# Optimization experiments

Measured on AMD Instinct MI355X. Metric: run time of the kernel, lower is better.

## Reference

```python
import jax, jax.numpy as jnp
import numpy as np

N = 50000      # nodes
E = 800000     # edges (before self loops)
F_IN = 50      # PPI num_features
H = 4          # heads
C = 64         # hidden per head
NC = 121       # PPI num_classes
NEG_SLOPE = 0.2


def setup_inputs() -> dict:
    key = jax.random.key(0)
    ks = jax.random.split(key, 20)
    p = lambda k, shape: (jax.random.normal(k, shape, jnp.float32) * 0.1)
    x0 = jax.random.normal(ks[0], (N, F_IN), jnp.float32)
    edge_index = jax.random.randint(ks[1], (2, E), 0, N, dtype=jnp.int64)
    return dict(
        x0=x0, edge_index=edge_index,
        W1=p(ks[2], (F_IN, H * C)), as1=p(ks[3], (H, C)), ad1=p(ks[4], (H, C)),
        res1=p(ks[5], (F_IN, H * C)), b1=jnp.zeros((H * C,), jnp.float32),
        W2=p(ks[6], (H * C, H * C)), as2=p(ks[7], (H, C)), ad2=p(ks[8], (H, C)),
        res2=p(ks[9], (H * C, H * C)), b2=jnp.zeros((H * C,), jnp.float32),
        W3=p(ks[10], (H * C, H * NC)), as3=p(ks[11], (H, NC)), ad3=p(ks[12], (H, NC)),
        res3=p(ks[13], (H * C, NC)), b3=jnp.zeros((NC,), jnp.float32),
    )


def _gat(x, src, dst, W, a_src, a_dst, resW, b, concat):
    """PyG-style GATConv with residual, self loops already in (src, dst)."""
    n = x.shape[0]
    heads, outc = a_src.shape
    h = (x @ W).reshape(n, heads, outc)                 # [N,H,C]
    al_s = (h * a_src).sum(-1)                          # [N,H]
    al_d = (h * a_dst).sum(-1)                          # [N,H]
    e = jax.nn.leaky_relu(al_s[src] + al_d[dst], NEG_SLOPE)  # [E,H]
    m = jax.ops.segment_max(e, dst, num_segments=n)     # stable softmax per dst
    ex = jnp.exp(e - m[dst])
    denom = jax.ops.segment_sum(ex, dst, num_segments=n)
    alpha = ex / denom[dst]                             # [E,H]
    out = jax.ops.segment_sum(h[src] * alpha[:, :, None], dst, num_segments=n)  # [N,H,C]
    out = out.reshape(n, heads * outc) if concat else out.mean(axis=1)
    return out + x @ resW + b


def reference(x0, edge_index,
              W1, as1, ad1, res1, b1,
              W2, as2, ad2, res2, b2,
              W3, as3, ad3, res3, b3):
    n = x0.shape[0]
    loop = jnp.arange(n, dtype=edge_index.dtype)        # add self loops (PyG default)
    src = jnp.concatenate([edge_index[0], loop])
    dst = jnp.concatenate([edge_index[1], loop])
    x1 = jax.nn.relu(_gat(x0, src, dst, W1, as1, ad1, res1, b1, True))
    x2 = jax.nn.relu(_gat(x1, src, dst, W2, as2, ad2, res2, b2, True))
    x3 = _gat(x2, src, dst, W3, as3, ad3, res3, b3, False)
    return x3
```

## Files before the change

kernel.cpp:

```cpp
#include <hip/hip_runtime.h>

#define NNODES 50000
#define NEDGES 800000
#define NTOT   (NEDGES + NNODES)
#define F_IN   50
#define KPAD1  64
#define HEADS  4
#define C1     64
#define HC1    256
#define NC     121
#define K1S    320
#define K3S    1280
#define N2S    512

typedef unsigned short ushort_t;
typedef __attribute__((ext_vector_type(4))) unsigned short ushort4_t;
typedef __attribute__((ext_vector_type(8))) unsigned short ushort8;
typedef __attribute__((ext_vector_type(8))) __bf16 bf16x8;
typedef __attribute__((ext_vector_type(4))) float f32x4;
typedef __attribute__((ext_vector_type(4))) int int4_t;

__device__ __forceinline__ ushort_t f2bf(float f) {
    union { float f; unsigned int u; } v; v.f = f;
    unsigned int u = v.u;
    return (ushort_t)((u + 0x7fffu + ((u >> 16) & 1u)) >> 16);
}
__device__ __forceinline__ float bf2f(ushort_t s) {
    union { unsigned int u; float f; } v; v.u = ((unsigned int)s) << 16;
    return v.f;
}
__device__ __forceinline__ float lrelu(float x) { return x > 0.f ? x : 0.2f * x; }
__device__ __forceinline__ f32x4 cvt4(ushort4_t v) {
    f32x4 r; r[0] = bf2f(v.x); r[1] = bf2f(v.y); r[2] = bf2f(v.z); r[3] = bf2f(v.w);
    return r;
}
__device__ __forceinline__ void wave_lds_sync() {
    asm volatile("s_waitcnt lgkmcnt(0)" ::: "memory");
}

__global__ void count_kernel(const int* __restrict__ ei, int* __restrict__ cnt) {
    int i = blockIdx.x * blockDim.x + threadIdx.x;
    if (i >= NTOT) return;
    int d = (i < NEDGES) ? ei[NEDGES + i] : (i - NEDGES);
    if ((unsigned)d >= NNODES) d = 0;
    atomicAdd(&cnt[d], 1);
}

#define SCB 256
__global__ __launch_bounds__(SCB)
void scan1_kernel(const int* __restrict__ cnt, int* __restrict__ incl,
                  int* __restrict__ bsums, int n) {
    __shared__ int buf[SCB];
    int b = blockIdx.x, tid = threadIdx.x;
    int i = b * SCB + tid;
    int v = (i < n) ? cnt[i] : 0;
    buf[tid] = v;
    __syncthreads();
    for (int off = 1; off < SCB; off <<= 1) {
        int t = (tid >= off) ? buf[tid - off] : 0;
        __syncthreads();
        buf[tid] += t;
        __syncthreads();
    }
    if (i < n) incl[i] = buf[tid];
    if (tid == SCB - 1) bsums[b] = buf[tid];
}

__global__ __launch_bounds__(SCB)
void scan2_kernel(int* __restrict__ bsums, int nb) {
    __shared__ int buf[SCB];
    int tid = threadIdx.x;
    int v = (tid < nb) ? bsums[tid] : 0;
    buf[tid] = v;
    __syncthreads();
    for (int off = 1; off < SCB; off <<= 1) {
        int t = (tid >= off) ? buf[tid - off] : 0;
        __syncthreads();
        buf[tid] += t;
        __syncthreads();
    }
    if (tid < nb) bsums[tid] = buf[tid] - v;
}

__global__ __launch_bounds__(SCB)
void scan3_kernel(const int* __restrict__ cnt, const int* __restrict__ incl,
                  const int* __restrict__ bsums, int* __restrict__ row_ptr,
                  int* __restrict__ cursor, int n) {
    int b = blockIdx.x, tid = threadIdx.x;
    int i = b * SCB + tid;
    if (i >= n) return;
    int e = bsums[b] + incl[i] - cnt[i];
    row_ptr[i] = e; cursor[i] = e;
    if (i == n - 1) row_ptr[n] = NTOT;
}

__global__ void scatter_kernel(const int* __restrict__ ei, int* __restrict__ cursor,
                               int* __restrict__ csr_src) {
    int i = blockIdx.x * blockDim.x + threadIdx.x;
    if (i >= NTOT) return;
    int s, d;
    if (i < NEDGES) { s = ei[i]; d = ei[NEDGES + i]; }
    else            { s = d = i - NEDGES; }
    if ((unsigned)d >= NNODES) d = 0;
    if ((unsigned)s >= NNODES) s = 0;
    int pos = atomicAdd(&cursor[d], 1);
    csr_src[pos] = s;
}

#define SZ_A (NNODES * KPAD1)
#define SZ_B (HC1 * K1S)
#define SZ_C (N2S * HC1)
#define SZ_D (N2S)
#define SZ_E (NC * K3S)
#define SZ_F (KPAD1 * 4)
#define SZ_G (HC1 * 4)
#define PREP_TOTAL (SZ_A + SZ_B + SZ_C + SZ_D + SZ_E + 2 * SZ_F + 4 * SZ_G)

__global__ __launch_bounds__(256)
void prep_kernel(const float* __restrict__ x0,
                 const float* __restrict__ W1, const float* __restrict__ res1,
                 const float* __restrict__ W2, const float* __restrict__ res2,
                 const float* __restrict__ W3, const float* __restrict__ res3,
                 const float* __restrict__ as1, const float* __restrict__ ad1,
                 const float* __restrict__ as2, const float* __restrict__ ad2,
                 const float* __restrict__ as3, const float* __restrict__ ad3,
                 const float* __restrict__ b2,
                 ushort_t* __restrict__ x0b, ushort_t* __restrict__ Bt1,
                 ushort_t* __restrict__ Bt2, ushort_t* __restrict__ Bt3,
                 float* __restrict__ bias512,
                 float* __restrict__ w_as1, float* __restrict__ w_ad1,
                 float* __restrict__ w_as2, float* __restrict__ w_ad2,
                 float* __restrict__ w_as3, float* __restrict__ w_ad3) {
    int i = blockIdx.x * 256 + threadIdx.x;
    if (i < SZ_A) {
        int m = i >> 6, k = i & 63;
        x0b[i] = (k < F_IN) ? f2bf(x0[(size_t)m * F_IN + k]) : (ushort_t)0;
        return;
    }
    i -= SZ_A;
    if (i < SZ_B) {
        int c = i / K1S, kk = i - c * K1S;
        float v = 0.f;
        if (kk < 256) {
            int h = kk >> 6, k = kk & 63;
            if (k < F_IN && (c >> 6) == h) v = W1[(size_t)k * HC1 + c];
        } else {
            int k = kk - 256;
            if (k < F_IN) v = res1[(size_t)k * HC1 + c];
        }
        Bt1[i] = f2bf(v);
        return;
    }
    i -= SZ_B;
    if (i < SZ_C) {
        int c = i / HC1, k = i - c * HC1;
        float v = (c < HC1) ? W2[(size_t)k * HC1 + c] : res2[(size_t)k * HC1 + (c - HC1)];
        Bt2[i] = f2bf(v);
        return;
    }
    i -= SZ_C;
    if (i < SZ_D) {
        bias512[i] = (i < HC1) ? 0.f : b2[i - HC1];
        return;
    }
    i -= SZ_D;
    if (i < SZ_E) {
        int c = i / K3S, kk = i - c * K3S;
        float v;
        if (kk < 1024) {
            int h = kk >> 8, k = kk & 255;
            v = 0.25f * W3[(size_t)k * (HEADS * NC) + h * NC + c];
        } else {
            int k = kk - 1024;
            v = res3[(size_t)k * NC + c];
        }
        Bt3[i] = f2bf(v);
        return;
    }
    i -= SZ_E;
    if (i < 2 * SZ_F) {
        const float* a = (i < SZ_F) ? as1 : ad1;
        float* w = (i < SZ_F) ? w_as1 : w_ad1;
        int ii = (i < SZ_F) ? i : i - SZ_F;
        int k = ii >> 2, h = ii & 3;
        float s = 0.f;
        if (k < F_IN)
            for (int c = 0; c < C1; ++c) s += W1[(size_t)k * HC1 + h * C1 + c] * a[h * C1 + c];
        w[ii] = s;
        return;
    }
    i -= 2 * SZ_F;
    {
        int grp = i / SZ_G, ii = i - grp * SZ_G;
        int k = ii >> 2, h = ii & 3;
        float s = 0.f;
        if (grp < 2) {
            const float* a = grp ? ad2 : as2;
            for (int c = 0; c < C1; ++c) s += W2[(size_t)k * HC1 + h * C1 + c] * a[h * C1 + c];
            (grp ? w_ad2 : w_as2)[ii] = s;
        } else {
            const float* a = (grp == 3) ? ad3 : as3;
            for (int c = 0; c < NC; ++c) s += W3[(size_t)k * (HEADS * NC) + h * NC + c] * a[h * NC + c];
            ((grp == 3) ? w_ad3 : w_as3)[ii] = s;
        }
    }
}

#define BM 128
#define BN 128
#define BK 64
#define LDP (BK + 8)

__global__ __launch_bounds__(256)
void gemm_mfma_kernel(const ushort_t* __restrict__ A1, int lda1,
                      const ushort_t* __restrict__ A2, int lda2, int Ksplit,
                      const ushort_t* __restrict__ Bt, const float* __restrict__ bias,
                      float* __restrict__ Cf, ushort_t* __restrict__ Cb,
                      int M, int N, int K, int relu) {
    __shared__ ushort_t As[BM * LDP];
    __shared__ ushort_t Bs[BN * LDP];
    int tid = threadIdx.x;
    int lane = tid & 63;
    int wid = tid >> 6;
    int wm = (wid & 1) * 64, wn = (wid >> 1) * 64;
    int l15 = lane & 15;
    int q8 = (lane >> 4) * 8;
    int m0 = blockIdx.y * BM, n0 = blockIdx.x * BN;

    f32x4 acc[4][4] = {};

    for (int k0 = 0; k0 < K; k0 += BK) {
        #pragma unroll
        for (int it = 0; it < 4; ++it) {
            int c = tid + it * 256;
            int row = c >> 3, c8 = c & 7;
            int k = k0 + c8 * 8;
            ushort8 va = (ushort8)0;
            int gm = m0 + row;
            if (gm < M) {
                if (k < Ksplit) va = *(const ushort8*)&A1[(size_t)gm * lda1 + k];
                else            va = *(const ushort8*)&A2[(size_t)gm * lda2 + (k - Ksplit)];
            }
            *(ushort8*)&As[row * LDP + c8 * 8] = va;
            ushort8 vb = (ushort8)0;
            int gn = n0 + row;
            if (gn < N) vb = *(const ushort8*)&Bt[(size_t)gn * K + k];
            *(ushort8*)&Bs[row * LDP + c8 * 8] = vb;
        }
        __syncthreads();
        #pragma unroll
        for (int kk = 0; kk < BK; kk += 32) {
            bf16x8 af[4], bfr[4];
            #pragma unroll
            for (int mi = 0; mi < 4; ++mi)
                af[mi] = *(const bf16x8*)&As[(wm + mi * 16 + l15) * LDP + kk + q8];
            #pragma unroll
            for (int ni = 0; ni < 4; ++ni)
                bfr[ni] = *(const bf16x8*)&Bs[(wn + ni * 16 + l15) * LDP + kk + q8];
            #pragma unroll
            for (int mi = 0; mi < 4; ++mi)
                #pragma unroll
                for (int ni = 0; ni < 4; ++ni)
                    acc[mi][ni] = __builtin_amdgcn_mfma_f32_16x16x32_bf16(
                        af[mi], bfr[ni], acc[mi][ni], 0, 0, 0);
        }
        __syncthreads();
    }

    #pragma unroll
    for (int mi = 0; mi < 4; ++mi) {
        int mbase = m0 + wm + mi * 16 + (lane >> 4) * 4;
        #pragma unroll
        for (int ni = 0; ni < 4; ++ni) {
            int ncol = n0 + wn + ni * 16 + l15;
            if (ncol >= N) continue;
            float bv = bias ? bias[ncol] : 0.f;
            #pragma unroll
            for (int r = 0; r < 4; ++r) {
                int m = mbase + r;
                if (m >= M) continue;
                float v = acc[mi][ni][r] + bv;
                if (relu) v = fmaxf(v, 0.f);
                if (Cf) Cf[(size_t)m * N + ncol] = v;
                else    Cb[(size_t)m * N + ncol] = f2bf(v);
            }
        }
    }
}

__global__ __launch_bounds__(256)
void logits_gemv_kernel(const ushort_t* __restrict__ X, int K,
                        const float* __restrict__ w_as, const float* __restrict__ w_ad,
                        float* __restrict__ als, float* __restrict__ ald) {
    int wid = threadIdx.x >> 6, lane = threadIdx.x & 63;
    int n = blockIdx.x * 4 + wid;
    float ps[HEADS] = {}, pd[HEADS] = {};
    for (int k0 = lane * 4; k0 < K; k0 += 256) {
        ushort4_t xv = *(const ushort4_t*)&X[(size_t)n * K + k0];
        float x[4] = {bf2f(xv.x), bf2f(xv.y), bf2f(xv.z), bf2f(xv.w)};
        #pragma unroll
        for (int j = 0; j < 4; ++j) {
            #pragma unroll
            for (int h = 0; h < HEADS; ++h) {
                ps[h] += x[j] * w_as[(k0 + j) * 4 + h];
                pd[h] += x[j] * w_ad[(k0 + j) * 4 + h];
            }
        }
    }
    #pragma unroll
    for (int off = 32; off; off >>= 1)
        #pragma unroll
        for (int h = 0; h < HEADS; ++h) {
            ps[h] += __shfl_xor(ps[h], off);
            pd[h] += __shfl_xor(pd[h], off);
        }
    if (lane == 0)
        #pragma unroll
        for (int h = 0; h < HEADS; ++h) {
            als[n * HEADS + h] = ps[h];
            ald[n * HEADS + h] = pd[h];
        }
}

#define E_CHUNK_NOMAX(ROWBYTES)                                               \
    int i = base + lane;                                                      \
    int nv = end - base; if (nv > 64) nv = 64;                                \
    if (i < end) {                                                            \
        int s = csr_src[i];                                                   \
        soffw[lane] = s * (ROWBYTES);                                         \
        f32x4 av = *(const f32x4*)&als[s * 4];                                \
        f32x4 e;                                                              \
        _Pragma("unroll")                                                     \
        for (int h = 0; h < HEADS; ++h) {                                     \
            e[h] = __expf(lrelu(av[h] + aldd[h]));                            \
            den4[h] += e[h];                                                  \
        }                                                                     \
        *(f32x4*)&sew[lane * 4] = e;                                          \
    }                                                                         \
    wave_lds_sync();

#define DEN_REDUCE                                                            \
    _Pragma("unroll")                                                         \
    for (int off = 32; off; off >>= 1)                                        \
        _Pragma("unroll")                                                     \
        for (int h = 0; h < HEADS; ++h)                                       \
            den4[h] += __shfl_xor(den4[h], off);

__global__ __launch_bounds__(256)
void agg1_kernel(const ushort_t* __restrict__ x0b,
                 const float* __restrict__ als, const float* __restrict__ ald,
                 const int* __restrict__ row_ptr, const int* __restrict__ csr_src,
                 ushort_t* __restrict__ aggx) {
    __shared__ int   soff[4][64];
    __shared__ float se[4][64 * 4];
    int wid = threadIdx.x >> 6, lane = threadIdx.x & 63;
    int d = blockIdx.x * 4 + wid;
    int* soffw = soff[wid];
    float* sew = se[wid];
    int beg = row_ptr[d], end = row_ptr[d + 1];
    f32x4 aldd = *(const f32x4*)&ald[d * 4];
    f32x4 den4 = (f32x4)0.f;
    f32x4 acc  = (f32x4)0.f;
    int lb = lane * 2;
    for (int base = beg; base < end; base += 64) {
        E_CHUNK_NOMAX(KPAD1 * 2)
        int j = 0;
        for (; j + 4 <= nv; j += 4) {
            int4_t o = *(const int4_t*)&soffw[j];
            f32x4 e0 = *(const f32x4*)&sew[j * 4];
            f32x4 e1 = *(const f32x4*)&sew[(j + 1) * 4];
            f32x4 e2 = *(const f32x4*)&sew[(j + 2) * 4];
            f32x4 e3 = *(const f32x4*)&sew[(j + 3) * 4];
            float x0v = bf2f(*(const ushort_t*)((const char*)x0b + o.x + lb));
            float x1v = bf2f(*(const ushort_t*)((const char*)x0b + o.y + lb));
            float x2v = bf2f(*(const ushort_t*)((const char*)x0b + o.z + lb));
            float x3v = bf2f(*(const ushort_t*)((const char*)x0b + o.w + lb));
            acc += e0 * x0v + e1 * x1v + e2 * x2v + e3 * x3v;
        }
        for (; j < nv; ++j) {
            int o = soffw[j];
            f32x4 e = *(const f32x4*)&sew[j * 4];
            float xv = bf2f(*(const ushort_t*)((const char*)x0b + o + lb));
            acc += e * xv;
        }
        wave_lds_sync();
    }
    DEN_REDUCE
    #pragma unroll
    for (int h = 0; h < HEADS; ++h)
        aggx[(size_t)d * HC1 + h * 64 + lane] = f2bf(acc[h] / den4[h]);
}

__global__ __launch_bounds__(256)
void agg2_kernel(const ushort_t* __restrict__ comb,
                 const float* __restrict__ als, const float* __restrict__ ald,
                 const int* __restrict__ row_ptr, const int* __restrict__ csr_src,
                 const float* __restrict__ w_as3, const float* __restrict__ w_ad3,
                 ushort_t* __restrict__ xnext,
                 float* __restrict__ als3, float* __restrict__ ald3) {
    __shared__ int   soff[4][64];
    __shared__ float se[4][64 * 4];
    int wid = threadIdx.x >> 6, lane = threadIdx.x & 63;
    int d = blockIdx.x * 4 + wid;
    int* soffw = soff[wid];
    float* sew = se[wid];
    int hh = lane >> 4;
    int beg = row_ptr[d], end = row_ptr[d + 1];
    f32x4 aldd = *(const f32x4*)&ald[d * 4];
    f32x4 den4 = (f32x4)0.f;
    f32x4 acc  = (f32x4)0.f;
    int lb = lane * 8;
    for (int base = beg; base < end; base += 64) {
        E_CHUNK_NOMAX(N2S * 2)
        int j = 0;
        for (; j + 4 <= nv; j += 4) {
            int4_t o = *(const int4_t*)&soffw[j];
            float e0 = sew[j * 4 + hh], e1 = sew[(j + 1) * 4 + hh];
            float e2 = sew[(j + 2) * 4 + hh], e3 = sew[(j + 3) * 4 + hh];
            f32x4 x0v = cvt4(*(const ushort4_t*)((const char*)comb + o.x + lb));
            f32x4 x1v = cvt4(*(const ushort4_t*)((const char*)comb + o.y + lb));
            f32x4 x2v = cvt4(*(const ushort4_t*)((const char*)comb + o.z + lb));
            f32x4 x3v = cvt4(*(const ushort4_t*)((const char*)comb + o.w + lb));
            acc += e0 * x0v + e1 * x1v + e2 * x2v + e3 * x3v;
        }
        for (; j < nv; ++j) {
            int o = soffw[j];
            float e = sew[j * 4 + hh];
            acc += e * cvt4(*(const ushort4_t*)((const char*)comb + o + lb));
        }
        wave_lds_sync();
    }
    DEN_REDUCE
    float r = 1.f / den4[hh];
    ushort4_t rv = *(const ushort4_t*)&comb[(size_t)d * N2S + 256 + lane * 4];
    f32x4 resv = cvt4(rv);
    f32x4 vout;
    #pragma unroll
    for (int c = 0; c < 4; ++c) vout[c] = fmaxf(acc[c] * r + resv[c], 0.f);
    ushort4_t o4;
    o4.x = f2bf(vout[0]); o4.y = f2bf(vout[1]); o4.z = f2bf(vout[2]); o4.w = f2bf(vout[3]);
    *(ushort4_t*)&xnext[(size_t)d * HC1 + lane * 4] = o4;
    f32x4 ps = (f32x4)0.f, pd = (f32x4)0.f;
    #pragma unroll
    for (int j = 0; j < 4; ++j) {
        f32x4 wsj = *(const f32x4*)&w_as3[(lane * 4 + j) * 4];
        f32x4 wdj = *(const f32x4*)&w_ad3[(lane * 4 + j) * 4];
        ps += vout[j] * wsj;
        pd += vout[j] * wdj;
    }
    #pragma unroll
    for (int off = 32; off; off >>= 1) {
        #pragma unroll
        for (int h = 0; h < HEADS; ++h) {
            ps[h] += __shfl_xor(ps[h], off);
            pd[h] += __shfl_xor(pd[h], off);
        }
    }
    if (lane == 0) {
        *(f32x4*)&als3[d * 4] = ps;
        *(f32x4*)&ald3[d * 4] = pd;
    }
}

__global__ __launch_bounds__(256)
void agg3_kernel(const ushort_t* __restrict__ x2b,
                 const float* __restrict__ als, const float* __restrict__ ald,
                 const int* __restrict__ row_ptr, const int* __restrict__ csr_src,
                 ushort_t* __restrict__ aggx) {
    __shared__ int   soff[4][64];
    __shared__ float se[4][64 * 4];
    int wid = threadIdx.x >> 6, lane = threadIdx.x & 63;
    int d = blockIdx.x * 4 + wid;
    int* soffw = soff[wid];
    float* sew = se[wid];
    int beg = row_ptr[d], end = row_ptr[d + 1];
    f32x4 aldd = *(const f32x4*)&ald[d * 4];
    f32x4 den4 = (f32x4)0.f;
    f32x4 acc[HEADS] = {};
    int lb = lane * 8;
    for (int base = beg; base < end; base += 64) {
        E_CHUNK_NOMAX(HC1 * 2)
        int j = 0;
        for (; j + 4 <= nv; j += 4) {
            int4_t o = *(const int4_t*)&soffw[j];
            f32x4 e0 = *(const f32x4*)&sew[j * 4];
            f32x4 e1 = *(const f32x4*)&sew[(j + 1) * 4];
            f32x4 e2 = *(const f32x4*)&sew[(j + 2) * 4];
            f32x4 e3 = *(const f32x4*)&sew[(j + 3) * 4];
            f32x4 x0v = cvt4(*(const ushort4_t*)((const char*)x2b + o.x + lb));
            f32x4 x1v = cvt4(*(const ushort4_t*)((const char*)x2b + o.y + lb));
            f32x4 x2v = cvt4(*(const ushort4_t*)((const char*)x2b + o.z + lb));
            f32x4 x3v = cvt4(*(const ushort4_t*)((const char*)x2b + o.w + lb));
            #pragma unroll
            for (int h = 0; h < HEADS; ++h)
                acc[h] += e0[h] * x0v + e1[h] * x1v + e2[h] * x2v + e3[h] * x3v;
        }
        for (; j < nv; ++j) {
            int o = soffw[j];
            f32x4 e = *(const f32x4*)&sew[j * 4];
            f32x4 xv = cvt4(*(const ushort4_t*)((const char*)x2b + o + lb));
            #pragma unroll
            for (int h = 0; h < HEADS; ++h) acc[h] += e[h] * xv;
        }
        wave_lds_sync();
    }
    DEN_REDUCE
    #pragma unroll
    for (int h = 0; h < HEADS; ++h) {
        float rd = 1.f / den4[h];
        ushort4_t o4;
        o4.x = f2bf(acc[h][0] * rd); o4.y = f2bf(acc[h][1] * rd);
        o4.z = f2bf(acc[h][2] * rd); o4.w = f2bf(acc[h][3] * rd);
        *(ushort4_t*)&aggx[(size_t)d * 1024 + h * HC1 + lane * 4] = o4;
    }
}

extern "C" void kernel_launch(void* const* d_in, const int* in_sizes, int n_in,
                              void* d_out, int out_size, void* d_ws, size_t ws_size,
                              hipStream_t stream) {
    const float* x0   = (const float*)d_in[0];
    const int*   ei   = (const int*)d_in[1];
    const float* W1   = (const float*)d_in[2];
    const float* as1  = (const float*)d_in[3];
    const float* ad1  = (const float*)d_in[4];
    const float* res1 = (const float*)d_in[5];
    const float* b1   = (const float*)d_in[6];
    const float* W2   = (const float*)d_in[7];
    const float* as2  = (const float*)d_in[8];
    const float* ad2  = (const float*)d_in[9];
    const float* res2 = (const float*)d_in[10];
    const float* b2   = (const float*)d_in[11];
    const float* W3   = (const float*)d_in[12];
    const float* as3  = (const float*)d_in[13];
    const float* ad3  = (const float*)d_in[14];
    const float* res3 = (const float*)d_in[15];
    const float* b3   = (const float*)d_in[16];

    char* p = (char*)d_ws;
    auto alloc = [&](size_t bytes) -> void* {
        void* r = (void*)p;
        p += (bytes + 255) & ~(size_t)255;
        return r;
    };
    int*      cnt     = (int*)alloc((size_t)NNODES * 4);
    int*      incl    = (int*)alloc((size_t)NNODES * 4);
    int*      bsums   = (int*)alloc((size_t)SCB * 4);
    int*      row_ptr = (int*)alloc((size_t)(NNODES + 1) * 4);
    int*      cursor  = (int*)alloc((size_t)NNODES * 4);
    int*      csr_src = (int*)alloc((size_t)NTOT * 4);
    float*    als     = (float*)alloc((size_t)NNODES * HEADS * 4);
    float*    ald     = (float*)alloc((size_t)NNODES * HEADS * 4);
    float*    als3    = (float*)alloc((size_t)NNODES * HEADS * 4);
    float*    ald3    = (float*)alloc((size_t)NNODES * HEADS * 4);
    ushort_t* x0b     = (ushort_t*)alloc((size_t)NNODES * KPAD1 * 2);
    ushort_t* x2      = (ushort_t*)alloc((size_t)NNODES * HC1 * 2);
    ushort_t* Bt1     = (ushort_t*)alloc((size_t)HC1 * K1S * 2);
    ushort_t* Bt2     = (ushort_t*)alloc((size_t)N2S * HC1 * 2);
    float*    bias512 = (float*)alloc((size_t)N2S * 4);
    ushort_t* Bt3     = (ushort_t*)alloc((size_t)NC * K3S * 2);
    float*    w_as1   = (float*)alloc((size_t)KPAD1 * 4 * 4);
    float*    w_ad1   = (float*)alloc((size_t)KPAD1 * 4 * 4);
    float*    w_as2   = (float*)alloc((size_t)HC1 * 4 * 4);
    float*    w_ad2   = (float*)alloc((size_t)HC1 * 4 * 4);
    float*    w_as3   = (float*)alloc((size_t)HC1 * 4 * 4);
    float*    w_ad3   = (float*)alloc((size_t)HC1 * 4 * 4);
    char*     big     = (char*)alloc((size_t)NNODES * 1024 * 2);
    ushort_t* aggx1   = (ushort_t*)big;
    ushort_t* x1      = (ushort_t*)(big + (size_t)NNODES * HC1 * 2);
    ushort_t* comb    = (ushort_t*)(big + (size_t)NNODES * HC1 * 4);
    ushort_t* aggx3   = (ushort_t*)big;

    hipMemsetAsync(cnt, 0, (size_t)NNODES * 4, stream);

    int tb = 256;
    int nscan = (NNODES + SCB - 1) / SCB;
    count_kernel<<<(NTOT + tb - 1) / tb, tb, 0, stream>>>(ei, cnt);
    scan1_kernel<<<nscan, SCB, 0, stream>>>(cnt, incl, bsums, NNODES);
    scan2_kernel<<<1, SCB, 0, stream>>>(bsums, nscan);
    scan3_kernel<<<nscan, SCB, 0, stream>>>(cnt, incl, bsums, row_ptr, cursor, NNODES);
    scatter_kernel<<<(NTOT + tb - 1) / tb, tb, 0, stream>>>(ei, cursor, csr_src);

    prep_kernel<<<(PREP_TOTAL + 255) / 256, 256, 0, stream>>>(
        x0, W1, res1, W2, res2, W3, res3, as1, ad1, as2, ad2, as3, ad3, b2,
        x0b, Bt1, Bt2, Bt3, bias512, w_as1, w_ad1, w_as2, w_ad2, w_as3, w_ad3);

    auto gemm = [&](const ushort_t* A1, int lda1, const ushort_t* A2, int lda2, int Ksplit,
                    const ushort_t* Bt, const float* bias,
                    float* Cf, ushort_t* Cb, int M, int Nn, int K, int relu) {
        dim3 g((Nn + BN - 1) / BN, (M + BM - 1) / BM);
        gemm_mfma_kernel<<<g, 256, 0, stream>>>(A1, lda1, A2, lda2, Ksplit, Bt, bias,
                                                Cf, Cb, M, Nn, K, relu);
    };

    int nagg = NNODES / 4;

    logits_gemv_kernel<<<nagg, 256, 0, stream>>>(x0b, KPAD1, w_as1, w_ad1, als, ald);
    agg1_kernel<<<nagg, 256, 0, stream>>>(x0b, als, ald, row_ptr, csr_src, aggx1);
    gemm(aggx1, HC1, x0b, KPAD1, HC1, Bt1, b1, nullptr, x1, NNODES, HC1, K1S, 1);

    gemm(x1, HC1, x1, HC1, HC1, Bt2, bias512, nullptr, comb, NNODES, N2S, HC1, 0);
    logits_gemv_kernel<<<nagg, 256, 0, stream>>>(x1, HC1, w_as2, w_ad2, als, ald);
    agg2_kernel<<<nagg, 256, 0, stream>>>(comb, als, ald, row_ptr, csr_src,
                                          w_as3, w_ad3, x2, als3, ald3);

    agg3_kernel<<<nagg, 256, 0, stream>>>(x2, als3, ald3, row_ptr, csr_src, aggx3);
    gemm(aggx3, 1024, x2, HC1, 1024, Bt3, b3, (float*)d_out, nullptr, NNODES, NC, K3S, 0);
}
```

Baseline: 640.7 us.

## Fuse independent setup kernels and make aggregation kernels grid-stride persistent

New measurement: 659.9 us. 1.03x slower.

```diff
diff --git a/kernel.cpp b/kernel.cpp
--- a/kernel.cpp
+++ b/kernel.cpp
@@ -38,8 +38,8 @@
     asm volatile("s_waitcnt lgkmcnt(0)" ::: "memory");
 }
 
-__global__ void count_kernel(const int* __restrict__ ei, int* __restrict__ cnt) {
-    int i = blockIdx.x * blockDim.x + threadIdx.x;
+__device__ __forceinline__ void count_body(int i, const int* __restrict__ ei,
+                                           int* __restrict__ cnt) {
     if (i >= NTOT) return;
     int d = (i < NEDGES) ? ei[NEDGES + i] : (i - NEDGES);
     if ((unsigned)d >= NNODES) d = 0;
@@ -94,9 +94,9 @@
     if (i == n - 1) row_ptr[n] = NTOT;
 }
 
-__global__ void scatter_kernel(const int* __restrict__ ei, int* __restrict__ cursor,
-                               int* __restrict__ csr_src) {
-    int i = blockIdx.x * blockDim.x + threadIdx.x;
+__device__ __forceinline__ void scatter_body(int i, const int* __restrict__ ei,
+                                             int* __restrict__ cursor,
+                                             int* __restrict__ csr_src) {
     if (i >= NTOT) return;
     int s, d;
     if (i < NEDGES) { s = ei[i]; d = ei[NEDGES + i]; }
@@ -115,9 +115,11 @@
 #define SZ_F (KPAD1 * 4)
 #define SZ_G (HC1 * 4)
 #define PREP_TOTAL (SZ_A + SZ_B + SZ_C + SZ_D + SZ_E + 2 * SZ_F + 4 * SZ_G)
-
-__global__ __launch_bounds__(256)
-void prep_kernel(const float* __restrict__ x0,
+#define PREP_BLK ((PREP_TOTAL + 255) / 256)
+#define CNT_BLK  ((NTOT + 255) / 256)
+
+__device__ void prep_body(int i,
+                 const float* __restrict__ x0,
                  const float* __restrict__ W1, const float* __restrict__ res1,
                  const float* __restrict__ W2, const float* __restrict__ res2,
                  const float* __restrict__ W3, const float* __restrict__ res3,
@@ -131,7 +133,6 @@
                  float* __restrict__ w_as1, float* __restrict__ w_ad1,
                  float* __restrict__ w_as2, float* __restrict__ w_ad2,
                  float* __restrict__ w_as3, float* __restrict__ w_ad3) {
-    int i = blockIdx.x * 256 + threadIdx.x;
     if (i < SZ_A) {
         int m = i >> 6, k = i & 63;
         x0b[i] = (k < F_IN) ? f2bf(x0[(size_t)m * F_IN + k]) : (ushort_t)0;
@@ -203,6 +204,32 @@
             for (int c = 0; c < NC; ++c) s += W3[(size_t)k * (HEADS * NC) + h * NC + c] * a[h * NC + c];
             ((grp == 3) ? w_ad3 : w_as3)[ii] = s;
         }
+    }
+}
+
+__global__ __launch_bounds__(256)
+void prep_count_kernel(const float* __restrict__ x0,
+                 const float* __restrict__ W1, const float* __restrict__ res1,
+                 const float* __restrict__ W2, const float* __restrict__ res2,
+                 const float* __restrict__ W3, const float* __restrict__ res3,
+                 const float* __restrict__ as1, const float* __restrict__ ad1,
+                 const float* __restrict__ as2, const float* __restrict__ ad2,
+                 const float* __restrict__ as3, const float* __restrict__ ad3,
+                 const float* __restrict__ b2,
+                 ushort_t* __restrict__ x0b, ushort_t* __restrict__ Bt1,
+                 ushort_t* __restrict__ Bt2, ushort_t* __restrict__ Bt3,
+                 float* __restrict__ bias512,
+                 float* __restrict__ w_as1, float* __restrict__ w_ad1,
+                 float* __restrict__ w_as2, float* __restrict__ w_ad2,
+                 float* __restrict__ w_as3, float* __restrict__ w_ad3,
+                 const int* __restrict__ ei, int* __restrict__ cnt) {
+    int b = blockIdx.x;
+    if (b < PREP_BLK) {
+        prep_body(b * 256 + threadIdx.x, x0, W1, res1, W2, res2, W3, res3,
+                  as1, ad1, as2, ad2, as3, ad3, b2, x0b, Bt1, Bt2, Bt3,
+                  bias512, w_as1, w_ad1, w_as2, w_ad2, w_as3, w_ad3);
+    } else {
+        count_body((b - PREP_BLK) * 256 + threadIdx.x, ei, cnt);
     }
 }
 
@@ -288,12 +315,10 @@
     }
 }
 
-__global__ __launch_bounds__(256)
-void logits_gemv_kernel(const ushort_t* __restrict__ X, int K,
+__device__ __forceinline__ void gemv_body(int n, int lane,
+                        const ushort_t* __restrict__ X, int K,
                         const float* __restrict__ w_as, const float* __restrict__ w_ad,
                         float* __restrict__ als, float* __restrict__ ald) {
-    int wid = threadIdx.x >> 6, lane = threadIdx.x & 63;
-    int n = blockIdx.x * 4 + wid;
     float ps[HEADS] = {}, pd[HEADS] = {};
     for (int k0 = lane * 4; k0 < K; k0 += 256) {
         ushort4_t xv = *(const ushort4_t*)&X[(size_t)n * K + k0];
@@ -320,6 +345,28 @@
             als[n * HEADS + h] = ps[h];
             ald[n * HEADS + h] = pd[h];
         }
+}
+
+__global__ __launch_bounds__(256)
+void logits_gemv_kernel(const ushort_t* __restrict__ X, int K,
+                        const float* __restrict__ w_as, const float* __restrict__ w_ad,
+                        float* __restrict__ als, float* __restrict__ ald) {
+    gemv_body(blockIdx.x * 4 + (threadIdx.x >> 6), threadIdx.x & 63, X, K, w_as, w_ad, als, ald);
+}
+
+#define GEMV_BLK (NNODES / 4)
+__global__ __launch_bounds__(256)
+void scatter_gemv1_kernel(const int* __restrict__ ei, int* __restrict__ cursor,
+                          int* __restrict__ csr_src,
+                          const ushort_t* __restrict__ X,
+                          const float* __restrict__ w_as, const float* __restrict__ w_ad,
+                          float* __restrict__ als, float* __restrict__ ald) {
+    int b = blockIdx.x;
+    if (b < GEMV_BLK) {
+        gemv_body(b * 4 + (threadIdx.x >> 6), threadIdx.x & 63, X, KPAD1, w_as, w_ad, als, ald);
+    } else {
+        scatter_body((b - GEMV_BLK) * 256 + threadIdx.x, ei, cursor, csr_src);
+    }
 }
 
 #define E_CHUNK_NOMAX(ROWBYTES)                                               \
@@ -346,6 +393,9 @@
         for (int h = 0; h < HEADS; ++h)                                       \
             den4[h] += __shfl_xor(den4[h], off);
 
+#define AGG_BLOCKS 2048
+#define AGG_WAVES  (AGG_BLOCKS * 4)
+
 __global__ __launch_bounds__(256)
 void agg1_kernel(const ushort_t* __restrict__ x0b,
                  const float* __restrict__ als, const float* __restrict__ ald,
@@ -354,41 +404,42 @@
     __shared__ int   soff[4][64];
     __shared__ float se[4][64 * 4];
     int wid = threadIdx.x >> 6, lane = threadIdx.x & 63;
-    int d = blockIdx.x * 4 + wid;
     int* soffw = soff[wid];
     float* sew = se[wid];
-    int beg = row_ptr[d], end = row_ptr[d + 1];
-    f32x4 aldd = *(const f32x4*)&ald[d * 4];
-    f32x4 den4 = (f32x4)0.f;
-    f32x4 acc  = (f32x4)0.f;
     int lb = lane * 2;
-    for (int base = beg; base < end; base += 64) {
-        E_CHUNK_NOMAX(KPAD1 * 2)
-        int j = 0;
-        for (; j + 4 <= nv; j += 4) {
-            int4_t o = *(const int4_t*)&soffw[j];
-            f32x4 e0 = *(const f32x4*)&sew[j * 4];
-            f32x4 e1 = *(const f32x4*)&sew[(j + 1) * 4];
-            f32x4 e2 = *(const f32x4*)&sew[(j + 2) * 4];
-            f32x4 e3 = *(const f32x4*)&sew[(j + 3) * 4];
-            float x0v = bf2f(*(const ushort_t*)((const char*)x0b + o.x + lb));
-            float x1v = bf2f(*(const ushort_t*)((const char*)x0b + o.y + lb));
-            float x2v = bf2f(*(const ushort_t*)((const char*)x0b + o.z + lb));
-            float x3v = bf2f(*(const ushort_t*)((const char*)x0b + o.w + lb));
-            acc += e0 * x0v + e1 * x1v + e2 * x2v + e3 * x3v;
-        }
-        for (; j < nv; ++j) {
-            int o = soffw[j];
-            f32x4 e = *(const f32x4*)&sew[j * 4];
-            float xv = bf2f(*(const ushort_t*)((const char*)x0b + o + lb));
-            acc += e * xv;
-        }
-        wave_lds_sync();
-    }
-    DEN_REDUCE
-    #pragma unroll
-    for (int h = 0; h < HEADS; ++h)
-        aggx[(size_t)d * HC1 + h * 64 + lane] = f2bf(acc[h] / den4[h]);
+    for (int d = blockIdx.x * 4 + wid; d < NNODES; d += AGG_WAVES) {
+        int beg = row_ptr[d], end = row_ptr[d + 1];
+        f32x4 aldd = *(const f32x4*)&ald[d * 4];
+        f32x4 den4 = (f32x4)0.f;
+        f32x4 acc  = (f32x4)0.f;
+        for (int base = beg; base < end; base += 64) {
+            E_CHUNK_NOMAX(KPAD1 * 2)
+            int j = 0;
+            for (; j + 4 <= nv; j += 4) {
+                int4_t o = *(const int4_t*)&soffw[j];
+                f32x4 e0 = *(const f32x4*)&sew[j * 4];
+                f32x4 e1 = *(const f32x4*)&sew[(j + 1) * 4];
+                f32x4 e2 = *(const f32x4*)&sew[(j + 2) * 4];
+                f32x4 e3 = *(const f32x4*)&sew[(j + 3) * 4];
+                float x0v = bf2f(*(const ushort_t*)((const char*)x0b + o.x + lb));
+                float x1v = bf2f(*(const ushort_t*)((const char*)x0b + o.y + lb));
+                float x2v = bf2f(*(const ushort_t*)((const char*)x0b + o.z + lb));
+                float x3v = bf2f(*(const ushort_t*)((const char*)x0b + o.w + lb));
+                acc += e0 * x0v + e1 * x1v + e2 * x2v + e3 * x3v;
+            }
+            for (; j < nv; ++j) {
+                int o = soffw[j];
+                f32x4 e = *(const f32x4*)&sew[j * 4];
+                float xv = bf2f(*(const ushort_t*)((const char*)x0b + o + lb));
+                acc += e * xv;
+            }
+            wave_lds_sync();
+        }
+        DEN_REDUCE
+        #pragma unroll
+        for (int h = 0; h < HEADS; ++h)
+            aggx[(size_t)d * HC1 + h * 64 + lane] = f2bf(acc[h] / den4[h]);
+    }
 }
 
 __global__ __launch_bounds__(256)
@@ -401,64 +452,66 @@
     __shared__ int   soff[4][64];
     __shared__ float se[4][64 * 4];
     int wid = threadIdx.x >> 6, lane = threadIdx.x & 63;
-    int d = blockIdx.x * 4 + wid;
     int* soffw = soff[wid];
     float* sew = se[wid];
     int hh = lane >> 4;
-    int beg = row_ptr[d], end = row_ptr[d + 1];
-    f32x4 aldd = *(const f32x4*)&ald[d * 4];
-    f32x4 den4 = (f32x4)0.f;
-    f32x4 acc  = (f32x4)0.f;
     int lb = lane * 8;
-    for (int base = beg; base < end; base += 64) {
-        E_CHUNK_NOMAX(N2S * 2)
-        int j = 0;
-        for (; j + 4 <= nv; j += 4) {
-            int4_t o = *(const int4_t*)&soffw[j];
-            float e0 = sew[j * 4 + hh], e1 = sew[(j + 1) * 4 + hh];
-            float e2 = sew[(j + 2) * 4 + hh], e3 = sew[(j + 3) * 4 + hh];
-            f32x4 x0v = cvt4(*(const ushort4_t*)((const char*)comb + o.x + lb));
-            f32x4 x1v = cvt4(*(const ushort4_t*)((const char*)comb + o.y + lb));
-            f32x4 x2v = cvt4(*(const ushort4_t*)((const char*)comb + o.z + lb));
-            f32x4 x3v = cvt4(*(const ushort4_t*)((const char*)comb + o.w + lb));
-            acc += e0 * x0v + e1 * x1v + e2 * x2v + e3 * x3v;
-        }
-        for (; j < nv; ++j) {
-            int o = soffw[j];
-            float e = sew[j * 4 + hh];
-            acc += e * cvt4(*(const ushort4_t*)((const char*)comb + o + lb));
-        }
-        wave_lds_sync();
-    }
-    DEN_REDUCE
-    float r = 1.f / den4[hh];
-    ushort4_t rv = *(const ushort4_t*)&comb[(size_t)d * N2S + 256 + lane * 4];
-    f32x4 resv = cvt4(rv);
-    f32x4 vout;
-    #pragma unroll
-    for (int c = 0; c < 4; ++c) vout[c] = fmaxf(acc[c] * r + resv[c], 0.f);
-    ushort4_t o4;
-    o4.x = f2bf(vout[0]); o4.y = f2bf(vout[1]); o4.z = f2bf(vout[2]); o4.w = f2bf(vout[3]);
-    *(ushort4_t*)&xnext[(size_t)d * HC1 + lane * 4] = o4;
-    f32x4 ps = (f32x4)0.f, pd = (f32x4)0.f;
-    #pragma unroll
-    for (int j = 0; j < 4; ++j) {
-        f32x4 wsj = *(const f32x4*)&w_as3[(lane * 4 + j) * 4];
-        f32x4 wdj = *(const f32x4*)&w_ad3[(lane * 4 + j) * 4];
-        ps += vout[j] * wsj;
-        pd += vout[j] * wdj;
-    }
-    #pragma unroll
-    for (int off = 32; off; off >>= 1) {
-        #pragma unroll
-        for (int h = 0; h < HEADS; ++h) {
-            ps[h] += __shfl_xor(ps[h], off);
-            pd[h] += __shfl_xor(pd[h], off);
-        }
-    }
-    if (lane == 0) {
-        *(f32x4*)&als3[d * 4] = ps;
-        *(f32x4*)&ald3[d * 4] = pd;
+    for (int d = blockIdx.x * 4 + wid; d < NNODES; d += AGG_WAVES) {
+        int beg = row_ptr[d], end = row_ptr[d + 1];
+        f32x4 aldd = *(const f32x4*)&ald[d * 4];
+        f32x4 den4 = (f32x4)0.f;
+        f32x4 acc  = (f32x4)0.f;
+        for (int base = beg; base < end; base += 64) {
+            E_CHUNK_NOMAX(N2S * 2)
+            int j = 0;
+            for (; j + 4 <= nv; j += 4) {
+                int4_t o = *(const int4_t*)&soffw[j];
+                float e0 = sew[j * 4 + hh], e1 = sew[(j + 1) * 4 + hh];
+                float e2 = sew[(j + 2) * 4 + hh], e3 = sew[(j + 3) * 4 + hh];
+                f32x4 x0v = cvt4(*(const ushort4_t*)((const char*)comb + o.x + lb));
+                f32x4 x1v = cvt4(*(const ushort4_t*)((const char*)comb + o.y + lb));
+                f32x4 x2v = cvt4(*(const ushort4_t*)((const char*)comb + o.z + lb));
+                f32x4 x3v = cvt4(*(const ushort4_t*)((const char*)comb + o.w + lb));
+                acc += e0 * x0v + e1 * x1v + e2 * x2v + e3 * x3v;
+            }
+            for (; j < nv; ++j) {
+                int o = soffw[j];
+                float e = sew[j * 4 + hh];
+                acc += e * cvt4(*(const ushort4_t*)((const char*)comb + o + lb));
+            }
+            wave_lds_sync();
+        }
+        DEN_REDUCE
+        float r = 1.f / den4[hh];
+        ushort4_t rv = *(const ushort4_t*)&comb[(size_t)d * N2S + 256 + lane * 4];
+        f32x4 resv = cvt4(rv);
+        f32x4 vout;
+        #pragma unroll
+        for (int c = 0; c < 4; ++c) vout[c] = fmaxf(acc[c] * r + resv[c], 0.f);
+        ushort4_t o4;
+        o4.x = f2bf(vout[0]); o4.y = f2bf(vout[1]);
+        o4.z = f2bf(vout[2]); o4.w = f2bf(vout[3]);
+        *(ushort4_t*)&xnext[(size_t)d * HC1 + lane * 4] = o4;
+        f32x4 ps = (f32x4)0.f, pd = (f32x4)0.f;
+        #pragma unroll
+        for (int j = 0; j < 4; ++j) {
+            f32x4 wsj = *(const f32x4*)&w_as3[(lane * 4 + j) * 4];
+            f32x4 wdj = *(const f32x4*)&w_ad3[(lane * 4 + j) * 4];
+            ps += vout[j] * wsj;
+            pd += vout[j] * wdj;
+        }
+        #pragma unroll
+        for (int off = 32; off; off >>= 1) {
+            #pragma unroll
+            for (int h = 0; h < HEADS; ++h) {
+                ps[h] += __shfl_xor(ps[h], off);
+                pd[h] += __shfl_xor(pd[h], off);
+            }
+        }
+        if (lane == 0) {
+            *(f32x4*)&als3[d * 4] = ps;
+            *(f32x4*)&ald3[d * 4] = pd;
+        }
     }
 }
 
@@ -470,48 +523,49 @@
     __shared__ int   soff[4][64];
     __shared__ float se[4][64 * 4];
     int wid = threadIdx.x >> 6, lane = threadIdx.x & 63;
-    int d = blockIdx.x * 4 + wid;
     int* soffw = soff[wid];
     float* sew = se[wid];
-    int beg = row_ptr[d], end = row_ptr[d + 1];
-    f32x4 aldd = *(const f32x4*)&ald[d * 4];
-    f32x4 den4 = (f32x4)0.f;
-    f32x4 acc[HEADS] = {};
     int lb = lane * 8;
-    for (int base = beg; base < end; base += 64) {
-        E_CHUNK_NOMAX(HC1 * 2)
-        int j = 0;
-        for (; j + 4 <= nv; j += 4) {
-            int4_t o = *(const int4_t*)&soffw[j];
-            f32x4 e0 = *(const f32x4*)&sew[j * 4];
-            f32x4 e1 = *(const f32x4*)&sew[(j + 1) * 4];
-            f32x4 e2 = *(const f32x4*)&sew[(j + 2) * 4];
-            f32x4 e3 = *(const f32x4*)&sew[(j + 3) * 4];
-            f32x4 x0v = cvt4(*(const ushort4_t*)((const char*)x2b + o.x + lb));
-            f32x4 x1v = cvt4(*(const ushort4_t*)((const char*)x2b + o.y + lb));
-            f32x4 x2v = cvt4(*(const ushort4_t*)((const char*)x2b + o.z + lb));
-            f32x4 x3v = cvt4(*(const ushort4_t*)((const char*)x2b + o.w + lb));
-            #pragma unroll
-            for (int h = 0; h < HEADS; ++h)
-                acc[h] += e0[h] * x0v + e1[h] * x1v + e2[h] * x2v + e3[h] * x3v;
-        }
-        for (; j < nv; ++j) {
-            int o = soffw[j];
-            f32x4 e = *(const f32x4*)&sew[j * 4];
-            f32x4 xv = cvt4(*(const ushort4_t*)((const char*)x2b + o + lb));
-            #pragma unroll
-            for (int h = 0; h < HEADS; ++h) acc[h] += e[h] * xv;
-        }
-        wave_lds_sync();
-    }
-    DEN_REDUCE
-    #pragma unroll
-    for (int h = 0; h < HEADS; ++h) {
-        float rd = 1.f / den4[h];
-        ushort4_t o4;
-        o4.x = f2bf(acc[h][0] * rd); o4.y = f2bf(acc[h][1] * rd);
-        o4.z = f2bf(acc[h][2] * rd); o4.w = f2bf(acc[h][3] * rd);
-        *(ushort4_t*)&aggx[(size_t)d * 1024 + h * HC1 + lane * 4] = o4;
+    for (int d = blockIdx.x * 4 + wid; d < NNODES; d += AGG_WAVES) {
+        int beg = row_ptr[d], end = row_ptr[d + 1];
+        f32x4 aldd = *(const f32x4*)&ald[d * 4];
+        f32x4 den4 = (f32x4)0.f;
+        f32x4 acc[HEADS] = {};
+        for (int base = beg; base < end; base += 64) {
+            E_CHUNK_NOMAX(HC1 * 2)
+            int j = 0;
+            for (; j + 4 <= nv; j += 4) {
+                int4_t o = *(const int4_t*)&soffw[j];
+                f32x4 e0 = *(const f32x4*)&sew[j * 4];
+                f32x4 e1 = *(const f32x4*)&sew[(j + 1) * 4];
+                f32x4 e2 = *(const f32x4*)&sew[(j + 2) * 4];
+                f32x4 e3 = *(const f32x4*)&sew[(j + 3) * 4];
+                f32x4 x0v = cvt4(*(const ushort4_t*)((const char*)x2b + o.x + lb));
+                f32x4 x1v = cvt4(*(const ushort4_t*)((const char*)x2b + o.y + lb));
+                f32x4 x2v = cvt4(*(const ushort4_t*)((const char*)x2b + o.z + lb));
+                f32x4 x3v = cvt4(*(const ushort4_t*)((const char*)x2b + o.w + lb));
+                #pragma unroll
+                for (int h = 0; h < HEADS; ++h)
+                    acc[h] += e0[h] * x0v + e1[h] * x1v + e2[h] * x2v + e3[h] * x3v;
+            }
+            for (; j < nv; ++j) {
+                int o = soffw[j];
+                f32x4 e = *(const f32x4*)&sew[j * 4];
+                f32x4 xv = cvt4(*(const ushort4_t*)((const char*)x2b + o + lb));
+                #pragma unroll
+                for (int h = 0; h < HEADS; ++h) acc[h] += e[h] * xv;
+            }
+            wave_lds_sync();
+        }
+        DEN_REDUCE
+        #pragma unroll
+        for (int h = 0; h < HEADS; ++h) {
+            float rdv = 1.f / den4[h];
+            ushort4_t o4;
+            o4.x = f2bf(acc[h][0] * rdv); o4.y = f2bf(acc[h][1] * rdv);
+            o4.z = f2bf(acc[h][2] * rdv); o4.w = f2bf(acc[h][3] * rdv);
+            *(ushort4_t*)&aggx[(size_t)d * 1024 + h * HC1 + lane * 4] = o4;
+        }
     }
 }
 
@@ -572,17 +626,17 @@
 
     hipMemsetAsync(cnt, 0, (size_t)NNODES * 4, stream);
 
-    int tb = 256;
     int nscan = (NNODES + SCB - 1) / SCB;
-    count_kernel<<<(NTOT + tb - 1) / tb, tb, 0, stream>>>(ei, cnt);
+
+    prep_count_kernel<<<PREP_BLK + CNT_BLK, 256, 0, stream>>>(
+        x0, W1, res1, W2, res2, W3, res3, as1, ad1, as2, ad2, as3, ad3, b2,
+        x0b, Bt1, Bt2, Bt3, bias512, w_as1, w_ad1, w_as2, w_ad2, w_as3, w_ad3,
+        ei, cnt);
     scan1_kernel<<<nscan, SCB, 0, stream>>>(cnt, incl, bsums, NNODES);
     scan2_kernel<<<1, SCB, 0, stream>>>(bsums, nscan);
     scan3_kernel<<<nscan, SCB, 0, stream>>>(cnt, incl, bsums, row_ptr, cursor, NNODES);
-    scatter_kernel<<<(NTOT + tb - 1) / tb, tb, 0, stream>>>(ei, cursor, csr_src);
-
-    prep_kernel<<<(PREP_TOTAL + 255) / 256, 256, 0, stream>>>(
-        x0, W1, res1, W2, res2, W3, res3, as1, ad1, as2, ad2, as3, ad3, b2,
-        x0b, Bt1, Bt2, Bt3, bias512, w_as1, w_ad1, w_as2, w_ad2, w_as3, w_ad3);
+    scatter_gemv1_kernel<<<GEMV_BLK + CNT_BLK, 256, 0, stream>>>(
+        ei, cursor, csr_src, x0b, w_as1, w_ad1, als, ald);
 
     auto gemm = [&](const ushort_t* A1, int lda1, const ushort_t* A2, int lda2, int Ksplit,
                     const ushort_t* Bt, const float* bias,
@@ -594,15 +648,14 @@
 
     int nagg = NNODES / 4;
 
-    logits_gemv_kernel<<<nagg, 256, 0, stream>>>(x0b, KPAD1, w_as1, w_ad1, als, ald);
-    agg1_kernel<<<nagg, 256, 0, stream>>>(x0b, als, ald, row_ptr, csr_src, aggx1);
+    agg1_kernel<<<AGG_BLOCKS, 256, 0, stream>>>(x0b, als, ald, row_ptr, csr_src, aggx1);
     gemm(aggx1, HC1, x0b, KPAD1, HC1, Bt1, b1, nullptr, x1, NNODES, HC1, K1S, 1);
 
     gemm(x1, HC1, x1, HC1, HC1, Bt2, bias512, nullptr, comb, NNODES, N2S, HC1, 0);
     logits_gemv_kernel<<<nagg, 256, 0, stream>>>(x1, HC1, w_as2, w_ad2, als, ald);
-    agg2_kernel<<<nagg, 256, 0, stream>>>(comb, als, ald, row_ptr, csr_src,
-                                          w_as3, w_ad3, x2, als3, ald3);
-
-    agg3_kernel<<<nagg, 256, 0, stream>>>(x2, als3, ald3, row_ptr, csr_src, aggx3);
+    agg2_kernel<<<AGG_BLOCKS, 256, 0, stream>>>(comb, als, ald, row_ptr, csr_src,
+                                                w_as3, w_ad3, x2, als3, ald3);
+
+    agg3_kernel<<<AGG_BLOCKS, 256, 0, stream>>>(x2, als3, ald3, row_ptr, csr_src, aggx3);
     gemm(aggx3, 1024, x2, HC1, 1024, Bt3, b3, (float*)d_out, nullptr, NNODES, NC, K3S, 0);
 }
```
